# Optimization experiments

Hardware: AMD Instinct MI355X
Metric: run time of the kernel (lower is better)

The kernel has to match this reference:

```python
import jax, jax.numpy as jnp
import numpy as np

B, T, H, L = 64, 512, 768, 9


def _crf_logZ(logits, transitions, seqlen):
    # forward algorithm; state freezes at t >= seqlen (tfa semantics)
    Tn = logits.shape[1]
    alpha0 = logits[:, 0]  # [B,L]
    valid = (jnp.arange(1, Tn)[None, :] < seqlen[:, None]).T  # [T-1,B]
    xs = (jnp.swapaxes(logits[:, 1:], 0, 1), valid)

    def step(alpha, inp):
        logit_t, v = inp
        new = jax.nn.logsumexp(alpha[:, :, None] + transitions[None], axis=1) + logit_t
        return jnp.where(v[:, None], new, alpha), None

    alphaT, _ = jax.lax.scan(step, alpha0, xs)
    return jax.nn.logsumexp(alphaT, axis=1)  # [B]


def _crf_score(logits, transitions, label, seqlen):
    Tn = logits.shape[1]
    seqmask = (jnp.arange(Tn)[None, :] < seqlen[:, None]).astype(logits.dtype)  # [B,T]
    unary = jnp.take_along_axis(logits, label[..., None], axis=2)[..., 0]
    unary = jnp.sum(unary * seqmask, axis=1)
    trans = transitions[label[:, :-1], label[:, 1:]]
    trans = jnp.sum(trans * seqmask[:, 1:], axis=1)
    return unary + trans  # [B]


def _viterbi(logits, transitions, seqlen):
    Tn, Ln = logits.shape[1], logits.shape[2]
    alpha0 = logits[:, 0]
    valid = (jnp.arange(1, Tn)[None, :] < seqlen[:, None]).T  # [T-1,B]
    xs = (jnp.swapaxes(logits[:, 1:], 0, 1), valid)
    idL = jnp.arange(Ln, dtype=jnp.int32)

    def step(alpha, inp):
        logit_t, v = inp
        scores = alpha[:, :, None] + transitions[None]  # [B,L,L]
        new = jnp.max(scores, axis=1) + logit_t
        bp = jnp.argmax(scores, axis=1).astype(jnp.int32)  # [B,L]
        alpha = jnp.where(v[:, None], new, alpha)
        bp = jnp.where(v[:, None], bp, idL[None, :])  # identity bp on padded steps
        return alpha, bp

    alphaT, bps = jax.lax.scan(step, alpha0, xs)  # bps: [T-1,B,L]
    last = jnp.argmax(alphaT, axis=1).astype(jnp.int32)  # [B]

    def back(tag, bp):
        prev = jnp.take_along_axis(bp, tag[:, None], axis=1)[:, 0]
        return prev, tag

    first, rest = jax.lax.scan(back, last, bps, reverse=True)
    tags = jnp.concatenate([first[None], rest], axis=0)  # [T,B]
    return jnp.swapaxes(tags, 0, 1)  # [B,T]


def setup_inputs() -> dict:
    key = jax.random.key(0)
    k = jax.random.split(key, 6)
    x = jax.random.normal(k[0], (B, T, H), dtype=jnp.float32)
    W = jax.random.truncated_normal(k[1], -2.0, 2.0, (H, L), dtype=jnp.float32) * 0.02
    b = jnp.zeros((L,), dtype=jnp.float32)
    lim = float(np.sqrt(6.0 / (L + L)))  # glorot_uniform
    transitions = jax.random.uniform(k[2], (L, L), dtype=jnp.float32, minval=-lim, maxval=lim)
    label = jax.random.randint(k[3], (B, T), 0, L, dtype=jnp.int32)
    seqlen = jax.random.randint(k[4], (B,), 1, T + 1, dtype=jnp.int32)
    mask = jnp.arange(T)[None, :] < seqlen[:, None]
    return {"x": x, "W": W, "b": b, "transitions": transitions, "label": label, "seqlen": seqlen, "mask": mask}


def reference(x, W, b, transitions, label, seqlen, mask):
    logits = jnp.einsum('bth,hl->btl', x, W) + b  # dense_ner
    ll = _crf_score(logits, transitions, label, seqlen) - _crf_logZ(logits, transitions, seqlen)
    loss = jnp.mean(-ll)
    vit = _viterbi(logits, transitions, seqlen)
    seqmask = (jnp.arange(logits.shape[1])[None, :] < seqlen[:, None]).astype(jnp.float32)
    accuracy = jnp.sum((vit == label).astype(jnp.float32) * seqmask) / jnp.sum(seqlen.astype(jnp.float32))
    tp = jnp.sum(((label > 0) & (vit == label)).astype(jnp.float32))
    tn = jnp.sum(((label > 0) & (vit != label)).astype(jnp.float32))
    fp = jnp.sum((mask & (label == 0) & (vit > 0)).astype(jnp.float32))
    return vit, tp, tn, fp, loss, accuracy
```

## Files before the change

kernel.cpp:

```cpp
#include <hip/hip_runtime.h>
#include <stdint.h>
#include <math.h>

#define NB 64
#define BT 512
#define NH 768
#define NL 9
#define PBT 528
#define PADW 772

__device__ __forceinline__ float rlane(float v, int i) {
    return __int_as_float(__builtin_amdgcn_readlane(__float_as_int(v), i));
}

template<int CTRL, int RM>
__device__ __forceinline__ float dppadd(float v) {
    const int t = __builtin_amdgcn_update_dpp(0, __float_as_int(v), CTRL, RM, 0xf, true);
    return v + __int_as_float(t);
}

__device__ __forceinline__ float wave_sum_dpp(float v) {
    v = dppadd<0x111, 0xf>(v);
    v = dppadd<0x112, 0xf>(v);
    v = dppadd<0x114, 0xf>(v);
    v = dppadd<0x118, 0xf>(v);
    v = dppadd<0x142, 0xa>(v);
    v = dppadd<0x143, 0xc>(v);
    return rlane(v, 63);
}

__global__ __launch_bounds__(256, 2) void gemm_kernel(
    const float* __restrict__ x, const float* __restrict__ W,
    const float* __restrict__ bias, float* __restrict__ logits)
{
    __shared__ float wT[NL * PADW];

    const int tid  = threadIdx.x;
    const int lane = tid & 63;

    for (int i = tid; i < NH * NL; i += 256) {
        const int h = i / NL, l = i - h * NL;
        wT[l * PADW + h] = W[i];
    }
    __syncthreads();

    float wr[3][NL][4];
#pragma unroll
    for (int k = 0; k < 3; ++k)
#pragma unroll
        for (int l = 0; l < NL; ++l) {
            const float4 w4 = *(const float4*)&wT[l * PADW + k * 256 + lane * 4];
            wr[k][l][0] = w4.x; wr[k][l][1] = w4.y;
            wr[k][l][2] = w4.z; wr[k][l][3] = w4.w;
        }
    const float bj = bias[lane < NL ? lane : 0];

    const int gwave = (blockIdx.x * blockDim.x + tid) >> 6;
    const int nw    = (gridDim.x * blockDim.x) >> 6;
    const int nrows = NB * BT;
    int row = gwave;
    if (row >= nrows) return;

    const float4* xr = (const float4*)(x + (size_t)row * NH);
    float4 a0 = xr[lane], a1 = xr[64 + lane], a2 = xr[128 + lane];

    while (true) {
        const int nrow = row + nw;
        float4 b0, b1, b2;
        if (nrow < nrows) {
            const float4* xn = (const float4*)(x + (size_t)nrow * NH);
            b0 = xn[lane]; b1 = xn[64 + lane]; b2 = xn[128 + lane];
        }

        float acc[NL];
#pragma unroll
        for (int l = 0; l < NL; ++l) {
            float s = a0.x * wr[0][l][0];
            s = fmaf(a0.y, wr[0][l][1], s);
            s = fmaf(a0.z, wr[0][l][2], s);
            s = fmaf(a0.w, wr[0][l][3], s);
            s = fmaf(a1.x, wr[1][l][0], s);
            s = fmaf(a1.y, wr[1][l][1], s);
            s = fmaf(a1.z, wr[1][l][2], s);
            s = fmaf(a1.w, wr[1][l][3], s);
            s = fmaf(a2.x, wr[2][l][0], s);
            s = fmaf(a2.y, wr[2][l][1], s);
            s = fmaf(a2.z, wr[2][l][2], s);
            s = fmaf(a2.w, wr[2][l][3], s);
            acc[l] = s;
        }
        float sum[NL];
#pragma unroll
        for (int l = 0; l < NL; ++l) sum[l] = wave_sum_dpp(acc[l]);
        float outv = sum[0];
#pragma unroll
        for (int l = 1; l < NL; ++l) outv = (lane == l) ? sum[l] : outv;
        if (lane < NL) logits[(size_t)row * NL + lane] = outv + bj;

        row = nrow;
        if (row >= nrows) break;
        a0 = b0; a1 = b1; a2 = b2;
    }
}

__global__ __launch_bounds__(256) void crf_kernel(
    const float* __restrict__ logits, const float* __restrict__ trans,
    const int* __restrict__ label, const int* __restrict__ seqlen,
    float* __restrict__ vit_out, float* __restrict__ stats)
{
    __shared__ __align__(16) float lg_lds[PBT * NL];
    __shared__ float    val_lds[BT * NL];
    __shared__ float    trans_lds[NL * NL];
    __shared__ uint8_t  bp_lds[(BT - 1) * NL];
    __shared__ uint64_t packed_lds[BT - 1];
    __shared__ uint8_t  vit_lds[BT];
    __shared__ float    xw[4][4];

    const int b    = blockIdx.x;
    const int tid  = threadIdx.x;
    const int lane = tid & 63;
    const int wv   = tid >> 6;
    const int sl   = seqlen[b];
    const float* lg  = logits + (size_t)b * BT * NL;
    const int*   lab = label + (size_t)b * BT;

    {
        const float4* src = (const float4*)lg;
        float4* dst = (float4*)lg_lds;
        for (int idx = tid; idx < BT * NL / 4; idx += 256) dst[idx] = src[idx];
        for (int idx = BT * NL + tid; idx < PBT * NL; idx += 256) lg_lds[idx] = 0.f;
        if (tid < NL * NL) trans_lds[tid] = trans[tid];
    }
    __syncthreads();

    if (wv == 0) {
        const int j = lane < NL ? lane : 0;
        float E[NL];
#pragma unroll
        for (int i = 0; i < NL; ++i) E[i] = __expf(trans_lds[i * NL + j]) * 0.125f;
        float A = __expf(lg_lds[j]);
        int lc = 0;
        for (int tb = 1; tb < BT + 8; tb += 8) {
            float P[8];
#pragma unroll
            for (int s = 0; s < 8; ++s) P[s] = __expf(lg_lds[(tb + s) * NL + j]);
#pragma unroll
            for (int s = 0; s < 8; ++s) {
                const int t = tb + s;
                const float r0 = rlane(A, 0), r1 = rlane(A, 1), r2 = rlane(A, 2),
                            r3 = rlane(A, 3), r4 = rlane(A, 4), r5 = rlane(A, 5),
                            r6 = rlane(A, 6), r7 = rlane(A, 7), r8 = rlane(A, 8);
                float p0 = r0 * E[0]; p0 = fmaf(r1, E[1], p0); p0 = fmaf(r2, E[2], p0);
                float p1 = r3 * E[3]; p1 = fmaf(r4, E[4], p1); p1 = fmaf(r5, E[5], p1);
                float p2 = r6 * E[6]; p2 = fmaf(r7, E[7], p2); p2 = fmaf(r8, E[8], p2);
                const float An = ((p0 + p1) + p2) * P[s];
                A = (t < sl) ? An : A;
            }
            const float m = fmaxf(fmaxf(
                fmaxf(fmaxf(rlane(A, 0), rlane(A, 1)), fmaxf(rlane(A, 2), rlane(A, 3))),
                fmaxf(fmaxf(rlane(A, 4), rlane(A, 5)), fmaxf(rlane(A, 6), rlane(A, 7)))),
                rlane(A, 8));
            const int ex = (int)((__float_as_uint(m) >> 23) & 0xFFu) - 126;
            const float sc = __uint_as_float((uint32_t)(127 - ex) << 23);
            A *= sc;
            lc += ex;
        }
        const float sum = ((rlane(A, 0) + rlane(A, 1)) + (rlane(A, 2) + rlane(A, 3))) +
                          ((rlane(A, 4) + rlane(A, 5)) + (rlane(A, 6) + rlane(A, 7))) +
                          rlane(A, 8);
        const float logZ = logf(sum) +
            ((float)lc + 3.0f * (float)(sl - 1)) * 0.6931471805599453f;
        if (lane == 0) stats[b * 8 + 1] = logZ;
    } else if (wv == 1) {
        const int j = lane < NL ? lane : 0;
        float tc[NL];
#pragma unroll
        for (int i = 0; i < NL; ++i) tc[i] = trans_lds[i * NL + j];
        float v = lg_lds[j];
        if (lane < NL) val_lds[j] = v;
        for (int tb = 1; tb < BT + 8; tb += 8) {
            float lv[8];
#pragma unroll
            for (int s = 0; s < 8; ++s) lv[s] = lg_lds[(tb + s) * NL + j];
#pragma unroll
            for (int s = 0; s < 8; ++s) {
                const int t = tb + s;
                const float r0 = rlane(v, 0), r1 = rlane(v, 1), r2 = rlane(v, 2),
                            r3 = rlane(v, 3), r4 = rlane(v, 4), r5 = rlane(v, 5),
                            r6 = rlane(v, 6), r7 = rlane(v, 7), r8 = rlane(v, 8);
                const float c0 = r0 + tc[0], c1 = r1 + tc[1], c2 = r2 + tc[2],
                            c3 = r3 + tc[3], c4 = r4 + tc[4], c5 = r5 + tc[5],
                            c6 = r6 + tc[6], c7 = r7 + tc[7], c8 = r8 + tc[8];
                const float m = fmaxf(fmaxf(fmaxf(fmaxf(c0, c1), c2),
                                            fmaxf(fmaxf(c3, c4), c5)),
                                      fmaxf(fmaxf(c6, c7), c8));
                const float nv = m + lv[s];
                v = (t < sl) ? nv : v;
                if (lane < NL && t < BT) val_lds[t * NL + lane] = v;
            }
        }
        const float r0 = rlane(v, 0), r1 = rlane(v, 1), r2 = rlane(v, 2),
                    r3 = rlane(v, 3), r4 = rlane(v, 4), r5 = rlane(v, 5),
                    r6 = rlane(v, 6), r7 = rlane(v, 7), r8 = rlane(v, 8);
        const float m = fmaxf(fmaxf(fmaxf(fmaxf(r0, r1), r2),
                                    fmaxf(fmaxf(r3, r4), r5)),
                              fmaxf(fmaxf(r6, r7), r8));
        const int last = (r0 == m) ? 0 : (r1 == m) ? 1 : (r2 == m) ? 2 :
                         (r3 == m) ? 3 : (r4 == m) ? 4 : (r5 == m) ? 5 :
                         (r6 == m) ? 6 : (r7 == m) ? 7 : 8;
        if (lane == 0) vit_lds[BT - 1] = (uint8_t)last;
    } else if (wv == 2) {
        float s = 0.f;
        for (int t = lane; t < BT; t += 64) {
            const int lb = lab[t];
            if (t < sl) {
                s += lg_lds[t * NL + lb];
                if (t >= 1) s += trans_lds[lab[t - 1] * NL + lb];
            }
        }
#pragma unroll
        for (int off = 32; off >= 1; off >>= 1) s += __shfl_xor(s, off, 64);
        if (lane == 0) stats[b * 8 + 0] = s;
    }
    __syncthreads();

    for (int idx = tid; idx < (BT - 1) * NL; idx += 256) {
        const int tm1 = idx / NL;
        const int jj  = idx - tm1 * NL;
        const int t   = tm1 + 1;
        int bi;
        if (t >= sl) bi = jj;
        else {
            float best = val_lds[tm1 * NL] + trans_lds[jj];
            bi = 0;
#pragma unroll
            for (int i = 1; i < NL; ++i) {
                const float c = val_lds[tm1 * NL + i] + trans_lds[i * NL + jj];
                if (c > best) { best = c; bi = i; }
            }
        }
        bp_lds[idx] = (uint8_t)bi;
    }
    __syncthreads();

    for (int r = tid; r < BT - 1; r += 256) {
        uint64_t p = 0;
#pragma unroll
        for (int i = 0; i < NL; ++i)
            p |= (uint64_t)bp_lds[r * NL + i] << (4 * i);
        packed_lds[r] = p;
    }
    __syncthreads();

    if (tid == 0) {
        int tag = vit_lds[BT - 1];
        for (int t = BT - 2; t >= 0; --t) {
            const uint64_t row = packed_lds[t];
            tag = (int)((row >> (4 * tag)) & 15u);
            vit_lds[t] = (uint8_t)tag;
        }
    }
    __syncthreads();

    float accv = 0.f, tpv = 0.f, tnv = 0.f, fpv = 0.f;
    for (int t = tid; t < BT; t += 256) {
        const int tg = vit_lds[t];
        const int lb = lab[t];
        const bool msk = t < sl;
        vit_out[(size_t)b * BT + t] = (float)tg;
        if (msk && tg == lb) accv += 1.f;
        if (lb > 0 && tg == lb) tpv += 1.f;
        if (lb > 0 && tg != lb) tnv += 1.f;
        if (msk && lb == 0 && tg > 0) fpv += 1.f;
    }
#pragma unroll
    for (int off = 32; off >= 1; off >>= 1) {
        accv += __shfl_xor(accv, off, 64);
        tpv  += __shfl_xor(tpv,  off, 64);
        tnv  += __shfl_xor(tnv,  off, 64);
        fpv  += __shfl_xor(fpv,  off, 64);
    }
    if (lane == 0) { xw[0][wv] = accv; xw[1][wv] = tpv; xw[2][wv] = tnv; xw[3][wv] = fpv; }
    __syncthreads();
    if (tid == 0) {
        stats[b * 8 + 2] = xw[0][0] + xw[0][1] + xw[0][2] + xw[0][3];
        stats[b * 8 + 3] = xw[1][0] + xw[1][1] + xw[1][2] + xw[1][3];
        stats[b * 8 + 4] = xw[2][0] + xw[2][1] + xw[2][2] + xw[2][3];
        stats[b * 8 + 5] = xw[3][0] + xw[3][1] + xw[3][2] + xw[3][3];
    }
}

__global__ __launch_bounds__(64) void finalize_kernel(
    const float* __restrict__ stats, const int* __restrict__ seqlen,
    float* __restrict__ out)
{
    const int lane = threadIdx.x;
    float score = stats[lane * 8 + 0];
    float logZ  = stats[lane * 8 + 1];
    float accv  = stats[lane * 8 + 2];
    float tpv   = stats[lane * 8 + 3];
    float tnv   = stats[lane * 8 + 4];
    float fpv   = stats[lane * 8 + 5];
    float nll   = logZ - score;
    float slf   = (float)seqlen[lane];
#pragma unroll
    for (int off = 32; off >= 1; off >>= 1) {
        nll  += __shfl_xor(nll,  off, 64);
        accv += __shfl_xor(accv, off, 64);
        tpv  += __shfl_xor(tpv,  off, 64);
        tnv  += __shfl_xor(tnv,  off, 64);
        fpv  += __shfl_xor(fpv,  off, 64);
        slf  += __shfl_xor(slf,  off, 64);
    }
    if (lane == 0) {
        out[NB * BT + 0] = tpv;
        out[NB * BT + 1] = tnv;
        out[NB * BT + 2] = fpv;
        out[NB * BT + 3] = nll / (float)NB;
        out[NB * BT + 4] = accv / slf;
    }
}

extern "C" void kernel_launch(void* const* d_in, const int* in_sizes, int n_in,
                              void* d_out, int out_size, void* d_ws, size_t ws_size,
                              hipStream_t stream)
{
    const float* x      = (const float*)d_in[0];
    const float* W      = (const float*)d_in[1];
    const float* bias   = (const float*)d_in[2];
    const float* trans  = (const float*)d_in[3];
    const int*   label  = (const int*)d_in[4];
    const int*   seqlen = (const int*)d_in[5];

    float* out    = (float*)d_out;
    float* logits = (float*)d_ws;
    float* stats  = logits + (size_t)NB * BT * NL;

    gemm_kernel<<<512, 256, 0, stream>>>(x, W, bias, logits);
    crf_kernel<<<NB, 256, 0, stream>>>(logits, trans, label, seqlen, out, stats);
    finalize_kernel<<<1, 64, 0, stream>>>(stats, seqlen, out);
}
```

Measured before the change: 212.7 us.

## Fuse finalize into CRF kernel, deepen GEMM prefetch, parallelize backpointer packing and backtrace

The GEMM now keeps two rows of x in flight instead of one, to hide more global-load latency. In the CRF kernel, each thread computes all 9 backpointers for one timestep and packs them straight into a 64-bit word, which removes the byte buffer and one barrier. The serial backtrace now reads packed rows from registers via readlane across a whole wave instead of from LDS on one thread. The separate finalize kernel is replaced by a last-block-done atomic counter, saving a launch, at the cost of a counter reset in the GEMM kernel and threadfence ordering.

```diff
diff --git a/kernel.cpp b/kernel.cpp
--- a/kernel.cpp
+++ b/kernel.cpp
@@ -11,6 +11,9 @@
 
 __device__ __forceinline__ float rlane(float v, int i) {
     return __int_as_float(__builtin_amdgcn_readlane(__float_as_int(v), i));
+}
+__device__ __forceinline__ uint32_t rlane_u(uint32_t v, int i) {
+    return (uint32_t)__builtin_amdgcn_readlane((int)v, i);
 }
 
 template<int CTRL, int RM>
@@ -31,8 +34,11 @@
 
 __global__ __launch_bounds__(256, 2) void gemm_kernel(
     const float* __restrict__ x, const float* __restrict__ W,
-    const float* __restrict__ bias, float* __restrict__ logits)
+    const float* __restrict__ bias, float* __restrict__ logits,
+    int* __restrict__ counter)
 {
+    if (blockIdx.x == 0 && threadIdx.x == 0) *counter = 0;
+
     __shared__ float wT[NL * PADW];
 
     const int tid  = threadIdx.x;
@@ -64,12 +70,19 @@
     const float4* xr = (const float4*)(x + (size_t)row * NH);
     float4 a0 = xr[lane], a1 = xr[64 + lane], a2 = xr[128 + lane];
 
+    int r1 = row + nw;
+    float4 b0{}, b1{}, b2{};
+    if (r1 < nrows) {
+        const float4* xn = (const float4*)(x + (size_t)r1 * NH);
+        b0 = xn[lane]; b1 = xn[64 + lane]; b2 = xn[128 + lane];
+    }
+
     while (true) {
-        const int nrow = row + nw;
-        float4 b0, b1, b2;
-        if (nrow < nrows) {
-            const float4* xn = (const float4*)(x + (size_t)nrow * NH);
-            b0 = xn[lane]; b1 = xn[64 + lane]; b2 = xn[128 + lane];
+        const int r2 = r1 + nw;
+        float4 c0{}, c1{}, c2{};
+        if (r2 < nrows) {
+            const float4* xn = (const float4*)(x + (size_t)r2 * NH);
+            c0 = xn[lane]; c1 = xn[64 + lane]; c2 = xn[128 + lane];
         }
 
         float acc[NL];
@@ -97,24 +110,27 @@
         for (int l = 1; l < NL; ++l) outv = (lane == l) ? sum[l] : outv;
         if (lane < NL) logits[(size_t)row * NL + lane] = outv + bj;
 
-        row = nrow;
-        if (row >= nrows) break;
+        if (r1 >= nrows) break;
         a0 = b0; a1 = b1; a2 = b2;
+        b0 = c0; b1 = c1; b2 = c2;
+        row = r1; r1 = r2;
     }
 }
 
 __global__ __launch_bounds__(256) void crf_kernel(
     const float* __restrict__ logits, const float* __restrict__ trans,
     const int* __restrict__ label, const int* __restrict__ seqlen,
-    float* __restrict__ vit_out, float* __restrict__ stats)
+    float* __restrict__ vit_out, float* __restrict__ stats,
+    int* __restrict__ counter)
 {
     __shared__ __align__(16) float lg_lds[PBT * NL];
     __shared__ float    val_lds[BT * NL];
     __shared__ float    trans_lds[NL * NL];
-    __shared__ uint8_t  bp_lds[(BT - 1) * NL];
     __shared__ uint64_t packed_lds[BT - 1];
     __shared__ uint8_t  vit_lds[BT];
     __shared__ float    xw[4][4];
+    __shared__ float    sh_score, sh_logZ;
+    __shared__ int      lastflag;
 
     const int b    = blockIdx.x;
     const int tid  = threadIdx.x;
@@ -156,10 +172,10 @@
                 const float An = ((p0 + p1) + p2) * P[s];
                 A = (t < sl) ? An : A;
             }
-            const float m = fmaxf(fmaxf(
-                fmaxf(fmaxf(rlane(A, 0), rlane(A, 1)), fmaxf(rlane(A, 2), rlane(A, 3))),
-                fmaxf(fmaxf(rlane(A, 4), rlane(A, 5)), fmaxf(rlane(A, 6), rlane(A, 7)))),
-                rlane(A, 8));
+            const float m = fmaxf(
+                fmaxf(fmaxf(fmaxf(rlane(A, 0), rlane(A, 1)), rlane(A, 2)),
+                      fmaxf(fmaxf(rlane(A, 3), rlane(A, 4)), rlane(A, 5))),
+                fmaxf(fmaxf(rlane(A, 6), rlane(A, 7)), rlane(A, 8)));
             const int ex = (int)((__float_as_uint(m) >> 23) & 0xFFu) - 126;
             const float sc = __uint_as_float((uint32_t)(127 - ex) << 23);
             A *= sc;
@@ -170,7 +186,7 @@
                           rlane(A, 8);
         const float logZ = logf(sum) +
             ((float)lc + 3.0f * (float)(sl - 1)) * 0.6931471805599453f;
-        if (lane == 0) stats[b * 8 + 1] = logZ;
+        if (lane == 0) sh_logZ = logZ;
     } else if (wv == 1) {
         const int j = lane < NL ? lane : 0;
         float tc[NL];
@@ -191,9 +207,9 @@
                 const float c0 = r0 + tc[0], c1 = r1 + tc[1], c2 = r2 + tc[2],
                             c3 = r3 + tc[3], c4 = r4 + tc[4], c5 = r5 + tc[5],
                             c6 = r6 + tc[6], c7 = r7 + tc[7], c8 = r8 + tc[8];
-                const float m = fmaxf(fmaxf(fmaxf(fmaxf(c0, c1), c2),
-                                            fmaxf(fmaxf(c3, c4), c5)),
-                                      fmaxf(fmaxf(c6, c7), c8));
+                const float m = fmaxf(
+                    fmaxf(fmaxf(fmaxf(c0, c1), c2), fmaxf(fmaxf(c3, c4), c5)),
+                    fmaxf(fmaxf(c6, c7), c8));
                 const float nv = m + lv[s];
                 v = (t < sl) ? nv : v;
                 if (lane < NL && t < BT) val_lds[t * NL + lane] = v;
@@ -202,9 +218,9 @@
         const float r0 = rlane(v, 0), r1 = rlane(v, 1), r2 = rlane(v, 2),
                     r3 = rlane(v, 3), r4 = rlane(v, 4), r5 = rlane(v, 5),
                     r6 = rlane(v, 6), r7 = rlane(v, 7), r8 = rlane(v, 8);
-        const float m = fmaxf(fmaxf(fmaxf(fmaxf(r0, r1), r2),
-                                    fmaxf(fmaxf(r3, r4), r5)),
-                              fmaxf(fmaxf(r6, r7), r8));
+        const float m = fmaxf(
+            fmaxf(fmaxf(fmaxf(r0, r1), r2), fmaxf(fmaxf(r3, r4), r5)),
+            fmaxf(fmaxf(r6, r7), r8));
         const int last = (r0 == m) ? 0 : (r1 == m) ? 1 : (r2 == m) ? 2 :
                          (r3 == m) ? 3 : (r4 == m) ? 4 : (r5 == m) ? 5 :
                          (r6 == m) ? 6 : (r7 == m) ? 7 : 8;
@@ -220,44 +236,58 @@
         }
 #pragma unroll
         for (int off = 32; off >= 1; off >>= 1) s += __shfl_xor(s, off, 64);
-        if (lane == 0) stats[b * 8 + 0] = s;
-    }
-    __syncthreads();
-
-    for (int idx = tid; idx < (BT - 1) * NL; idx += 256) {
-        const int tm1 = idx / NL;
-        const int jj  = idx - tm1 * NL;
-        const int t   = tm1 + 1;
-        int bi;
-        if (t >= sl) bi = jj;
-        else {
-            float best = val_lds[tm1 * NL] + trans_lds[jj];
-            bi = 0;
-#pragma unroll
-            for (int i = 1; i < NL; ++i) {
-                const float c = val_lds[tm1 * NL + i] + trans_lds[i * NL + jj];
-                if (c > best) { best = c; bi = i; }
-            }
-        }
-        bp_lds[idx] = (uint8_t)bi;
-    }
-    __syncthreads();
-
-    for (int r = tid; r < BT - 1; r += 256) {
-        uint64_t p = 0;
-#pragma unroll
-        for (int i = 0; i < NL; ++i)
-            p |= (uint64_t)bp_lds[r * NL + i] << (4 * i);
-        packed_lds[r] = p;
-    }
-    __syncthreads();
-
-    if (tid == 0) {
+        if (lane == 0) sh_score = s;
+    }
+    __syncthreads();
+
+    for (int tm1 = tid; tm1 < BT - 1; tm1 += 256) {
+        const int t = tm1 + 1;
+        uint64_t p;
+        if (t >= sl) {
+            p = 0x876543210ull;
+        } else {
+            float v[NL];
+#pragma unroll
+            for (int i = 0; i < NL; ++i) v[i] = val_lds[tm1 * NL + i];
+            p = 0;
+#pragma unroll
+            for (int jj = 0; jj < NL; ++jj) {
+                float best = v[0] + trans_lds[jj];
+                int bi = 0;
+#pragma unroll
+                for (int i = 1; i < NL; ++i) {
+                    const float c = v[i] + trans_lds[i * NL + jj];
+                    if (c > best) { best = c; bi = i; }
+                }
+                p |= (uint64_t)bi << (4 * jj);
+            }
+        }
+        packed_lds[tm1] = p;
+    }
+    __syncthreads();
+
+    if (wv == 0) {
+        uint32_t plo[8], phi[8];
+#pragma unroll
+        for (int r = 0; r < 8; ++r) {
+            const int t = r * 64 + lane;
+            uint64_t v = 0;
+            if (t < BT - 1) v = packed_lds[t];
+            plo[r] = (uint32_t)v;
+            phi[r] = (uint32_t)(v >> 32);
+        }
         int tag = vit_lds[BT - 1];
-        for (int t = BT - 2; t >= 0; --t) {
-            const uint64_t row = packed_lds[t];
-            tag = (int)((row >> (4 * tag)) & 15u);
-            vit_lds[t] = (uint8_t)tag;
+#pragma unroll
+        for (int r = 7; r >= 0; --r) {
+            const int lhi = (r == 7) ? 62 : 63;
+#pragma unroll 4
+            for (int l = lhi; l >= 0; --l) {
+                const uint32_t lo = rlane_u(plo[r], l);
+                const uint32_t hi = rlane_u(phi[r], l);
+                const uint32_t w  = (tag & 8) ? hi : lo;
+                tag = (int)((w >> ((4 * tag) & 31)) & 15u);
+                if (lane == 0) vit_lds[r * 64 + l] = (uint8_t)tag;
+            }
         }
     }
     __syncthreads();
@@ -282,42 +312,47 @@
     }
     if (lane == 0) { xw[0][wv] = accv; xw[1][wv] = tpv; xw[2][wv] = tnv; xw[3][wv] = fpv; }
     __syncthreads();
+
     if (tid == 0) {
+        stats[b * 8 + 0] = sh_score;
+        stats[b * 8 + 1] = sh_logZ;
         stats[b * 8 + 2] = xw[0][0] + xw[0][1] + xw[0][2] + xw[0][3];
         stats[b * 8 + 3] = xw[1][0] + xw[1][1] + xw[1][2] + xw[1][3];
         stats[b * 8 + 4] = xw[2][0] + xw[2][1] + xw[2][2] + xw[2][3];
         stats[b * 8 + 5] = xw[3][0] + xw[3][1] + xw[3][2] + xw[3][3];
-    }
-}
-
-__global__ __launch_bounds__(64) void finalize_kernel(
-    const float* __restrict__ stats, const int* __restrict__ seqlen,
-    float* __restrict__ out)
-{
-    const int lane = threadIdx.x;
-    float score = stats[lane * 8 + 0];
-    float logZ  = stats[lane * 8 + 1];
-    float accv  = stats[lane * 8 + 2];
-    float tpv   = stats[lane * 8 + 3];
-    float tnv   = stats[lane * 8 + 4];
-    float fpv   = stats[lane * 8 + 5];
-    float nll   = logZ - score;
-    float slf   = (float)seqlen[lane];
-#pragma unroll
-    for (int off = 32; off >= 1; off >>= 1) {
-        nll  += __shfl_xor(nll,  off, 64);
-        accv += __shfl_xor(accv, off, 64);
-        tpv  += __shfl_xor(tpv,  off, 64);
-        tnv  += __shfl_xor(tnv,  off, 64);
-        fpv  += __shfl_xor(fpv,  off, 64);
-        slf  += __shfl_xor(slf,  off, 64);
-    }
-    if (lane == 0) {
-        out[NB * BT + 0] = tpv;
-        out[NB * BT + 1] = tnv;
-        out[NB * BT + 2] = fpv;
-        out[NB * BT + 3] = nll / (float)NB;
-        out[NB * BT + 4] = accv / slf;
+        __threadfence();
+        const int done = atomicAdd(counter, 1);
+        lastflag = (done == NB - 1);
+    }
+    __syncthreads();
+
+    if (lastflag && tid < 64) {
+        __threadfence();
+        const int l = tid;
+        float score = stats[l * 8 + 0];
+        float logZ  = stats[l * 8 + 1];
+        float accs  = stats[l * 8 + 2];
+        float tps   = stats[l * 8 + 3];
+        float tns   = stats[l * 8 + 4];
+        float fps   = stats[l * 8 + 5];
+        float nll   = logZ - score;
+        float slf   = (float)seqlen[l];
+#pragma unroll
+        for (int off = 32; off >= 1; off >>= 1) {
+            nll  += __shfl_xor(nll,  off, 64);
+            accs += __shfl_xor(accs, off, 64);
+            tps  += __shfl_xor(tps,  off, 64);
+            tns  += __shfl_xor(tns,  off, 64);
+            fps  += __shfl_xor(fps,  off, 64);
+            slf  += __shfl_xor(slf,  off, 64);
+        }
+        if (l == 0) {
+            vit_out[NB * BT + 0] = tps;
+            vit_out[NB * BT + 1] = tns;
+            vit_out[NB * BT + 2] = fps;
+            vit_out[NB * BT + 3] = nll / (float)NB;
+            vit_out[NB * BT + 4] = accs / slf;
+        }
     }
 }
 
@@ -332,11 +367,11 @@
     const int*   label  = (const int*)d_in[4];
     const int*   seqlen = (const int*)d_in[5];
 
-    float* out    = (float*)d_out;
-    float* logits = (float*)d_ws;
-    float* stats  = logits + (size_t)NB * BT * NL;
-
-    gemm_kernel<<<512, 256, 0, stream>>>(x, W, bias, logits);
-    crf_kernel<<<NB, 256, 0, stream>>>(logits, trans, label, seqlen, out, stats);
-    finalize_kernel<<<1, 64, 0, stream>>>(stats, seqlen, out);
-}
+    float* out     = (float*)d_out;
+    float* logits  = (float*)d_ws;
+    float* stats   = logits + (size_t)NB * BT * NL;
+    int*   counter = (int*)(stats + NB * 8);
+
+    gemm_kernel<<<512, 256, 0, stream>>>(x, W, bias, logits, counter);
+    crf_kernel<<<NB, 256, 0, stream>>>(logits, trans, label, seqlen, out, stats, counter);
+}
```

Result: slower. 221.6 us (+4.2%).
